# Optimization experiments

Measured on AMD Instinct MI355X. Metric: run time of the kernel, lower is better.

Reference implementation:

```python
import jax, jax.numpy as jnp
import numpy as np

N_EMBD = 384
NUM_HEADS = 6
HEAD_SIZE = 64


def setup_inputs() -> dict:
    key = jax.random.key(0)
    k1, k2, k3, k4 = jax.random.split(key, 4)
    B, T = 32, 1024
    x = jax.random.normal(k1, (B, T, N_EMBD), dtype=jnp.float32)
    # torch Linear(n_embd, 3*n_embd, bias=False): store as [in, out]
    s_attn = 1.0 / np.sqrt(N_EMBD)
    W_attn = jax.random.uniform(k2, (N_EMBD, 3 * N_EMBD), dtype=jnp.float32, minval=-s_attn, maxval=s_attn)
    W_proj = jax.random.uniform(k3, (N_EMBD, N_EMBD), dtype=jnp.float32, minval=-s_attn, maxval=s_attn)
    b_proj = jax.random.uniform(k4, (N_EMBD,), dtype=jnp.float32, minval=-s_attn, maxval=s_attn)
    return {"x": x, "W_attn": W_attn, "W_proj": W_proj, "b_proj": b_proj}


def reference(x, W_attn, W_proj, b_proj):
    B, T, C = x.shape
    H, D = NUM_HEADS, HEAD_SIZE
    qkv = x @ W_attn                      # [B, T, 3C]
    q, k, v = jnp.split(qkv, 3, axis=2)   # each [B, T, C]
    # [B, H, T, D]
    q = q.reshape(B, T, H, D).transpose(0, 2, 1, 3)
    k = k.reshape(B, T, H, D).transpose(0, 2, 1, 3)
    v = v.reshape(B, T, H, D).transpose(0, 2, 1, 3)
    scale = 1.0 / jnp.sqrt(jnp.asarray(D, dtype=x.dtype))
    scores = jnp.einsum("bhqd,bhkd->bhqk", q, k) * scale  # [B, H, T, T]
    causal = jnp.tril(jnp.ones((T, T), dtype=bool))
    scores = jnp.where(causal, scores, jnp.asarray(-jnp.inf, dtype=scores.dtype))
    attn = jax.nn.softmax(scores, axis=-1)
    y = jnp.einsum("bhqk,bhkd->bhqd", attn, v)             # [B, H, T, D]
    y = y.transpose(0, 2, 1, 3).reshape(B, T, C)
    # dropout is inactive in eval mode
    return y @ W_proj + b_proj
```

## Files before the change

### kernel.cpp

```cpp
#include <hip/hip_runtime.h>
#include <hip/hip_bf16.h>

#define DEV __device__ __forceinline__

typedef __attribute__((ext_vector_type(4))) float f32x4;
typedef __bf16 bf16x8 __attribute__((ext_vector_type(8)));

static DEV unsigned short f2bf(float f) {
    union { float f; unsigned u; } x; x.f = f;
    unsigned r = x.u + 0x7fffu + ((x.u >> 16) & 1u);
    return (unsigned short)(r >> 16);
}

static DEV f32x4 zero4() { f32x4 v; v[0] = 0.f; v[1] = 0.f; v[2] = 0.f; v[3] = 0.f; return v; }

#define GL1(p) ((const __attribute__((address_space(1))) void*)(p))
#define LDS3(p) ((__attribute__((address_space(3))) void*)(p))


__global__ __launch_bounds__(256) void k_prep(
    const float* __restrict__ x, unsigned short* __restrict__ xb,
    const float* __restrict__ Wa, unsigned short* __restrict__ WaT,
    const float* __restrict__ Wp, unsigned short* __restrict__ WpT)
{
    int i = blockIdx.x * 256 + threadIdx.x;
    if (i < 3145728) {
        float4 v = reinterpret_cast<const float4*>(x)[i];
        ushort4 o;
        o.x = f2bf(v.x); o.y = f2bf(v.y); o.z = f2bf(v.z); o.w = f2bf(v.w);
        reinterpret_cast<ushort4*>(xb)[i] = o;
    } else if (i < 3145728 + 442368) {
        int j = i - 3145728;
        int n = j / 384, k = j - n * 384;
        WaT[j] = f2bf(Wa[(size_t)k * 1152 + n]);
    } else if (i < 3145728 + 442368 + 147456) {
        int j = i - (3145728 + 442368);
        int n = j / 384, k = j - n * 384;
        WpT[j] = f2bf(Wp[(size_t)k * 384 + n]);
    }
}


template <int SWAP>
static DEV void gemm_mainloop(
    const unsigned short* __restrict__ A,
    const unsigned short* __restrict__ B,
    int m0, int n0, int tid,
    f32x4 (&acc)[4][4],
    unsigned short (&lA)[128][64], unsigned short (&lB)[128][64])
{
    const int K = 384;
    const int w = tid >> 6, lane = tid & 63;
    const int wm = (w >> 1) * 64, wn = (w & 1) * 64;
    const int lr = lane & 15, lg = lane >> 4;
    const int lrow = lane >> 3;
    const int lcol = ((lane & 7) ^ lrow) * 8;

    for (int kb = 0; kb < K; kb += 64) {
        __syncthreads();
#pragma unroll
        for (int c = 0; c < 4; ++c) {
            int rb = (w * 4 + c) * 8;
            __builtin_amdgcn_global_load_lds(GL1(&A[(size_t)(m0 + rb + lrow) * K + kb + lcol]),
                                             LDS3(&lA[rb][0]), 16, 0, 0);
            __builtin_amdgcn_global_load_lds(GL1(&B[(size_t)(n0 + rb + lrow) * K + kb + lcol]),
                                             LDS3(&lB[rb][0]), 16, 0, 0);
        }
        __syncthreads();

        bf16x8 af[4][2], bfr[4][2];
#pragma unroll
        for (int kc = 0; kc < 2; ++kc) {
#pragma unroll
            for (int t = 0; t < 4; ++t) {
                int ga = ((kc * 4 + lg) ^ (lr & 7)) * 8;
                af[t][kc]  = *(const bf16x8*)&lA[wm + t * 16 + lr][ga];
                bfr[t][kc] = *(const bf16x8*)&lB[wn + t * 16 + lr][ga];
            }
        }
#pragma unroll
        for (int kc = 0; kc < 2; ++kc)
#pragma unroll
            for (int mt = 0; mt < 4; ++mt)
#pragma unroll
                for (int nt = 0; nt < 4; ++nt)
                    acc[mt][nt] = SWAP
                        ? __builtin_amdgcn_mfma_f32_16x16x32_bf16(bfr[nt][kc], af[mt][kc], acc[mt][nt], 0, 0, 0)
                        : __builtin_amdgcn_mfma_f32_16x16x32_bf16(af[mt][kc], bfr[nt][kc], acc[mt][nt], 0, 0, 0);
    }
}


__global__ __launch_bounds__(256) void k_gemm_qkv(
    const unsigned short* __restrict__ A,
    const unsigned short* __restrict__ B,
    unsigned short* __restrict__ Qb, unsigned short* __restrict__ Kb,
    unsigned short* __restrict__ Vb)
{
    __shared__ unsigned short lA[128][64];
    __shared__ unsigned short lB[128][64];

    const int bid = blockIdx.x;
    const int xcd = bid & 7, s = bid >> 3;
    const int mi = xcd * 32 + s / 9;
    const int cj = s % 9;
    const int m0 = mi * 128, n0 = cj * 128;

    const int tid = threadIdx.x;
    const int w = tid >> 6, lane = tid & 63;
    const int wm = (w >> 1) * 64, wn = (w & 1) * 64;
    const int lr = lane & 15, lg = lane >> 4;

    f32x4 acc[4][4];
#pragma unroll
    for (int i = 0; i < 4; i++)
#pragma unroll
        for (int j = 0; j < 4; j++) acc[i][j] = zero4();

    if (cj < 6) {
        gemm_mainloop<1>(A, B, m0, n0, tid, acc, lA, lB);
        const int which = cj / 3;
#pragma unroll
        for (int mt = 0; mt < 4; ++mt) {
            int row = m0 + wm + mt * 16 + lr;
            int bb = row >> 10, tloc = row & 1023;
#pragma unroll
            for (int nt = 0; nt < 4; ++nt) {
                int col = n0 + wn + nt * 16 + lg * 4;
                int c = col - which * 384;
                int hh = c >> 6, d0 = c & 63;
                size_t bh = (size_t)bb * 6 + hh;
                int kc = (d0 >> 5) & 1;
                int ln = (tloc & 15) + 16 * ((d0 >> 3) & 3);
                int e0 = d0 & 7;
                union { __bf16 h4[4]; uint2 u; } pk;
                if (which == 0) {
#pragma unroll
                    for (int r = 0; r < 4; ++r)
                        pk.h4[r] = (__bf16)(acc[mt][nt][r] * 0.18033688f);
                    int qt = tloc >> 5, fmt = (tloc >> 4) & 1;
                    *(uint2*)&Qb[((((bh * 32 + qt) * 2 + fmt) * 2 + kc) * 64 + ln) * 8 + e0] = pk.u;
                } else {
#pragma unroll
                    for (int r = 0; r < 4; ++r)
                        pk.h4[r] = (__bf16)acc[mt][nt][r];
                    int ktt = tloc >> 6, fnt = (tloc >> 4) & 3;
                    *(uint2*)&Kb[((((bh * 16 + ktt) * 4 + fnt) * 2 + kc) * 64 + ln) * 8 + e0] = pk.u;
                }
            }
        }
    } else {
        gemm_mainloop<0>(A, B, m0, n0, tid, acc, lA, lB);
#pragma unroll
        for (int nt = 0; nt < 4; ++nt) {
            int col = n0 + wn + nt * 16 + lr;
            int c = col - 768;
            int hh = c >> 6, d = c & 63;
            int fnt = d >> 4;
#pragma unroll
            for (int mt = 0; mt < 4; ++mt) {
                int row0 = m0 + wm + mt * 16 + lg * 4;
                int bb = row0 >> 10, t0 = row0 & 1023;
                size_t bh = (size_t)bb * 6 + hh;
                int ktt = t0 >> 6, kc = (t0 >> 5) & 1, e0 = t0 & 7;
                int ln = (d & 15) + 16 * ((t0 >> 3) & 3);
                union { __bf16 h4[4]; uint2 u; } pk;
#pragma unroll
                for (int r = 0; r < 4; ++r)
                    pk.h4[r] = (__bf16)acc[mt][nt][r];
                *(uint2*)&Vb[((((bh * 16 + ktt) * 4 + fnt) * 2 + kc) * 64 + ln) * 8 + e0] = pk.u;
            }
        }
    }
}


__global__ __launch_bounds__(256) void k_gemm_proj(
    const unsigned short* __restrict__ A,
    const unsigned short* __restrict__ B,
    const float* __restrict__ bias, float* __restrict__ Out)
{
    __shared__ unsigned short lA[128][64];
    __shared__ unsigned short lB[128][64];

    const int bid = blockIdx.x;
    const int xcd = bid & 7, s = bid >> 3;
    const int mi = xcd * 32 + s / 3;
    const int cj = s % 3;
    const int m0 = mi * 128, n0 = cj * 128;

    const int tid = threadIdx.x;
    const int w = tid >> 6, lane = tid & 63;
    const int wm = (w >> 1) * 64, wn = (w & 1) * 64;
    const int lr = lane & 15, lg = lane >> 4;

    f32x4 acc[4][4];
#pragma unroll
    for (int i = 0; i < 4; i++)
#pragma unroll
        for (int j = 0; j < 4; j++) acc[i][j] = zero4();

    gemm_mainloop<1>(A, B, m0, n0, tid, acc, lA, lB);

#pragma unroll
    for (int mt = 0; mt < 4; ++mt) {
        int row = m0 + wm + mt * 16 + lr;
#pragma unroll
        for (int nt = 0; nt < 4; ++nt) {
            int col = n0 + wn + nt * 16 + lg * 4;
            f32x4 bv = *(const f32x4*)&bias[col];
            f32x4 ov;
#pragma unroll
            for (int r = 0; r < 4; ++r) ov[r] = acc[mt][nt][r] + bv[r];
            *(f32x4*)&Out[(size_t)row * 384 + col] = ov;
        }
    }
}


template <int NTM, bool MASK>
static DEV void attn_qtile(
    const bf16x8 (&kf)[4][2], const bf16x8 (&vf)[4][2],
    const bf16x8 (&qf)[2][2], f32x4 (&o)[2][4], float (&ls)[2],
    unsigned short* lPw, int kt, int qw, int lr, int lg)
{
    constexpr int KCM = NTM / 2;

    f32x4 st[2][NTM];
#pragma unroll
    for (int mt = 0; mt < 2; ++mt)
#pragma unroll
        for (int nt = 0; nt < NTM; ++nt) st[mt][nt] = zero4();

    __builtin_amdgcn_s_setprio(1);
#pragma unroll
    for (int kc = 0; kc < 2; ++kc)
#pragma unroll
        for (int mt = 0; mt < 2; ++mt)
#pragma unroll
            for (int nt = 0; nt < NTM; ++nt)
                st[mt][nt] = __builtin_amdgcn_mfma_f32_16x16x32_bf16(kf[nt][kc], qf[mt][kc], st[mt][nt], 0, 0, 0);
    __builtin_amdgcn_s_setprio(0);

#pragma unroll
    for (int mt = 0; mt < 2; ++mt) {
#pragma unroll
        for (int nt = 0; nt < NTM; ++nt) {
            union { __bf16 hh[4]; uint2 u; } pk;
            float e[4];
#pragma unroll
            for (int r = 0; r < 4; ++r) {
                float ev = __builtin_amdgcn_exp2f(st[mt][nt][r]);
                if (MASK) {
                    int kg = kt * 64 + nt * 16 + lg * 4 + r;
                    int qg = qw + mt * 16 + lr;
                    if (kg > qg) ev = 0.f;
                }
                e[r] = ev;
                pk.hh[r] = (__bf16)ev;
            }
            ls[mt] += (e[0] + e[1]) + (e[2] + e[3]);
            int ln2 = lr + 16 * ((nt & 1) * 2 + (lg >> 1));
            *(uint2*)&lPw[(mt * 2 + (nt >> 1)) * 512 + ln2 * 8 + (lg & 1) * 4] = pk.u;
        }
    }

    bf16x8 pf[2][KCM];
#pragma unroll
    for (int mt = 0; mt < 2; ++mt)
#pragma unroll
        for (int kc = 0; kc < KCM; ++kc)
            pf[mt][kc] = *(const bf16x8*)&lPw[(mt * 2 + kc) * 512 + (lr + 16 * lg) * 8];

    __builtin_amdgcn_s_setprio(1);
#pragma unroll
    for (int mt = 0; mt < 2; ++mt)
#pragma unroll
        for (int nt = 0; nt < 4; ++nt)
#pragma unroll
            for (int kc = 0; kc < KCM; ++kc)
                o[mt][nt] = __builtin_amdgcn_mfma_f32_16x16x32_bf16(vf[nt][kc], pf[mt][kc], o[mt][nt], 0, 0, 0);
    __builtin_amdgcn_s_setprio(0);
}

static DEV void attn_out(const f32x4 (&o)[2][4], const float (&ls)[2],
                         int qw, int b, int h, int lr, int lg,
                         unsigned short* __restrict__ Y)
{
    float inv[2];
#pragma unroll
    for (int mt = 0; mt < 2; ++mt) {
        float s = ls[mt];
        s += __shfl_xor(s, 16);
        s += __shfl_xor(s, 32);
        inv[mt] = 1.0f / s;
    }
#pragma unroll
    for (int mt = 0; mt < 2; ++mt) {
#pragma unroll
        for (int nt = 0; nt < 4; ++nt) {
            union { __bf16 h4[4]; uint2 u; } pk;
#pragma unroll
            for (int r = 0; r < 4; ++r) pk.h4[r] = (__bf16)(o[mt][nt][r] * inv[mt]);
            *(uint2*)&Y[((size_t)b * 1024 + qw + mt * 16 + lr) * 384 + h * 64 + nt * 16 + lg * 4] = pk.u;
        }
    }
}

__global__ __launch_bounds__(256, 2) void k_attn(
    const unsigned short* __restrict__ Qf,
    const unsigned short* __restrict__ Kf,
    const unsigned short* __restrict__ Vf,
    unsigned short* __restrict__ Y)
{
    __shared__ unsigned short lK[2][4096];
    __shared__ unsigned short lV[2][4096];
    __shared__ unsigned short lPf[4][2048];

    const int tid = threadIdx.x;
    const int w = tid >> 6, lane = tid & 63;
    const int lr = lane & 15, lg = lane >> 4;
    const int bh = blockIdx.x;
    const int pg = 3 - blockIdx.y;
    const int p = 4 * pg + w;
    const int qtA = 2 * p, qtB = 2 * p + 1;
    const int qwA = qtA * 32, qwB = qtB * 32;
    const int nkt = p + 1;
    const int nsteps = 4 * pg + 4;
    const int b = bh / 6, h = bh - b * 6;

    const unsigned short* Kbh = Kf + (size_t)bh * 65536;
    const unsigned short* Vbh = Vf + (size_t)bh * 65536;

    bf16x8 qfA[2][2], qfB[2][2];
#pragma unroll
    for (int mt = 0; mt < 2; ++mt)
#pragma unroll
        for (int kc = 0; kc < 2; ++kc) {
            qfA[mt][kc] = *(const bf16x8*)&Qf[((((size_t)bh * 32 + qtA) * 2 + mt) * 2 + kc) * 512 + lane * 8];
            qfB[mt][kc] = *(const bf16x8*)&Qf[((((size_t)bh * 32 + qtB) * 2 + mt) * 2 + kc) * 512 + lane * 8];
        }

    f32x4 oA[2][4], oB[2][4];
    float lsA[2] = {0.f, 0.f}, lsB[2] = {0.f, 0.f};
#pragma unroll
    for (int mt = 0; mt < 2; ++mt)
#pragma unroll
        for (int nt = 0; nt < 4; ++nt) { oA[mt][nt] = zero4(); oB[mt][nt] = zero4(); }

#pragma unroll
    for (int i = 0; i < 2; ++i) {
        __builtin_amdgcn_global_load_lds(GL1(Kbh + (size_t)w * 1024 + i * 512 + lane * 8),
                                         LDS3(&lK[0][w * 1024 + i * 512]), 16, 0, 0);
        __builtin_amdgcn_global_load_lds(GL1(Vbh + (size_t)w * 1024 + i * 512 + lane * 8),
                                         LDS3(&lV[0][w * 1024 + i * 512]), 16, 0, 0);
    }

    for (int kt = 0; kt < nsteps; ++kt) {
        __syncthreads();
        if (kt + 1 < nsteps) {
            int nb = (kt + 1) & 1;
#pragma unroll
            for (int i = 0; i < 2; ++i) {
                __builtin_amdgcn_global_load_lds(GL1(Kbh + (size_t)(kt + 1) * 4096 + w * 1024 + i * 512 + lane * 8),
                                                 LDS3(&lK[nb][w * 1024 + i * 512]), 16, 0, 0);
                __builtin_amdgcn_global_load_lds(GL1(Vbh + (size_t)(kt + 1) * 4096 + w * 1024 + i * 512 + lane * 8),
                                                 LDS3(&lV[nb][w * 1024 + i * 512]), 16, 0, 0);
            }
        }
        if (kt < nkt) {
            const unsigned short* lKt = lK[kt & 1];
            const unsigned short* lVt = lV[kt & 1];

            bf16x8 kf[4][2], vf[4][2];
#pragma unroll
            for (int nt = 0; nt < 4; ++nt)
#pragma unroll
                for (int kc = 0; kc < 2; ++kc) {
                    kf[nt][kc] = *(const bf16x8*)&lKt[(nt * 2 + kc) * 512 + lane * 8];
                    vf[nt][kc] = *(const bf16x8*)&lVt[(nt * 2 + kc) * 512 + lane * 8];
                }

            if (kt == nkt - 1) {
                attn_qtile<2, true>(kf, vf, qfA, oA, lsA, lPf[w], kt, qwA, lr, lg);
                attn_qtile<4, true>(kf, vf, qfB, oB, lsB, lPf[w], kt, qwB, lr, lg);
            } else {
                attn_qtile<4, false>(kf, vf, qfA, oA, lsA, lPf[w], kt, qwA, lr, lg);
                attn_qtile<4, false>(kf, vf, qfB, oB, lsB, lPf[w], kt, qwB, lr, lg);
            }
        }
    }

    attn_out(oA, lsA, qwA, b, h, lr, lg, Y);
    attn_out(oB, lsB, qwB, b, h, lr, lg, Y);
}


extern "C" void kernel_launch(void* const* d_in, const int* in_sizes, int n_in,
                              void* d_out, int out_size, void* d_ws, size_t ws_size,
                              hipStream_t stream)
{
    const float* x  = (const float*)d_in[0];
    const float* Wa = (const float*)d_in[1];
    const float* Wp = (const float*)d_in[2];
    const float* bp = (const float*)d_in[3];
    float* out = (float*)d_out;

    char* ws = (char*)d_ws;
    unsigned short* xb  = (unsigned short*)(ws);
    unsigned short* WaT = (unsigned short*)(ws + 25165824);
    unsigned short* WpT = (unsigned short*)(ws + 26050560);
    unsigned short* Qb  = (unsigned short*)(ws + 26345472);
    unsigned short* Kb  = (unsigned short*)(ws + 51511296);
    unsigned short* Vtb = (unsigned short*)(ws + 76677120);

    k_prep<<<14592, 256, 0, stream>>>(x, xb, Wa, WaT, Wp, WpT);
    k_gemm_qkv<<<2304, 256, 0, stream>>>(xb, WaT, Qb, Kb, Vtb);
    k_attn<<<dim3(192, 4), 256, 0, stream>>>(Qb, Kb, Vtb, xb);
    k_gemm_proj<<<768, 256, 0, stream>>>(xb, WpT, bp, out);
}
```

Before: 126.8 us.

## Pair light and heavy causal query groups per attention block for load balance

The attention kernel now launches half as many blocks. Each block runs two phases: one over query group p and one over the mirrored group 15-p, so every block does about the same causal work. This is meant to remove the tail imbalance where blocks over late query tiles process many more key tiles than blocks over early ones. In exchange each block runs longer and serially, there are fewer blocks to hide latency, and an extra barrier and pipeline restart sit between the phases.

```diff
diff --git a/kernel.cpp b/kernel.cpp
--- a/kernel.cpp
+++ b/kernel.cpp
@@ -307,6 +307,85 @@
     }
 }
 
+static DEV void attn_phase(
+    int p, int nstage, int w, int lane, int b, int h, int bh,
+    const unsigned short* __restrict__ Qf,
+    const unsigned short* __restrict__ Kbh,
+    const unsigned short* __restrict__ Vbh,
+    unsigned short* __restrict__ Y,
+    unsigned short (&lK)[2][4096], unsigned short (&lV)[2][4096],
+    unsigned short* lPw)
+{
+    const int lr = lane & 15, lg = lane >> 4;
+    const int qtA = 2 * p, qtB = 2 * p + 1;
+    const int qwA = qtA * 32, qwB = qtB * 32;
+    const int nkt = p + 1;
+
+    bf16x8 qfA[2][2], qfB[2][2];
+#pragma unroll
+    for (int mt = 0; mt < 2; ++mt)
+#pragma unroll
+        for (int kc = 0; kc < 2; ++kc) {
+            qfA[mt][kc] = *(const bf16x8*)&Qf[((((size_t)bh * 32 + qtA) * 2 + mt) * 2 + kc) * 512 + lane * 8];
+            qfB[mt][kc] = *(const bf16x8*)&Qf[((((size_t)bh * 32 + qtB) * 2 + mt) * 2 + kc) * 512 + lane * 8];
+        }
+
+    f32x4 oA[2][4], oB[2][4];
+    float lsA[2] = {0.f, 0.f}, lsB[2] = {0.f, 0.f};
+#pragma unroll
+    for (int mt = 0; mt < 2; ++mt)
+#pragma unroll
+        for (int nt = 0; nt < 4; ++nt) { oA[mt][nt] = zero4(); oB[mt][nt] = zero4(); }
+
+    __syncthreads();
+
+#pragma unroll
+    for (int i = 0; i < 2; ++i) {
+        __builtin_amdgcn_global_load_lds(GL1(Kbh + (size_t)w * 1024 + i * 512 + lane * 8),
+                                         LDS3(&lK[0][w * 1024 + i * 512]), 16, 0, 0);
+        __builtin_amdgcn_global_load_lds(GL1(Vbh + (size_t)w * 1024 + i * 512 + lane * 8),
+                                         LDS3(&lV[0][w * 1024 + i * 512]), 16, 0, 0);
+    }
+
+    for (int kt = 0; kt < nstage; ++kt) {
+        __syncthreads();
+        if (kt + 1 < nstage) {
+            int nb = (kt + 1) & 1;
+#pragma unroll
+            for (int i = 0; i < 2; ++i) {
+                __builtin_amdgcn_global_load_lds(GL1(Kbh + (size_t)(kt + 1) * 4096 + w * 1024 + i * 512 + lane * 8),
+                                                 LDS3(&lK[nb][w * 1024 + i * 512]), 16, 0, 0);
+                __builtin_amdgcn_global_load_lds(GL1(Vbh + (size_t)(kt + 1) * 4096 + w * 1024 + i * 512 + lane * 8),
+                                                 LDS3(&lV[nb][w * 1024 + i * 512]), 16, 0, 0);
+            }
+        }
+        if (kt < nkt) {
+            const unsigned short* lKt = lK[kt & 1];
+            const unsigned short* lVt = lV[kt & 1];
+
+            bf16x8 kf[4][2], vf[4][2];
+#pragma unroll
+            for (int nt = 0; nt < 4; ++nt)
+#pragma unroll
+                for (int kc = 0; kc < 2; ++kc) {
+                    kf[nt][kc] = *(const bf16x8*)&lKt[(nt * 2 + kc) * 512 + lane * 8];
+                    vf[nt][kc] = *(const bf16x8*)&lVt[(nt * 2 + kc) * 512 + lane * 8];
+                }
+
+            if (kt == nkt - 1) {
+                attn_qtile<2, true>(kf, vf, qfA, oA, lsA, lPw, kt, qwA, lr, lg);
+                attn_qtile<4, true>(kf, vf, qfB, oB, lsB, lPw, kt, qwB, lr, lg);
+            } else {
+                attn_qtile<4, false>(kf, vf, qfA, oA, lsA, lPw, kt, qwA, lr, lg);
+                attn_qtile<4, false>(kf, vf, qfB, oB, lsB, lPw, kt, qwB, lr, lg);
+            }
+        }
+    }
+
+    attn_out(oA, lsA, qwA, b, h, lr, lg, Y);
+    attn_out(oB, lsB, qwB, b, h, lr, lg, Y);
+}
+
 __global__ __launch_bounds__(256, 2) void k_attn(
     const unsigned short* __restrict__ Qf,
     const unsigned short* __restrict__ Kf,
@@ -319,80 +398,16 @@
 
     const int tid = threadIdx.x;
     const int w = tid >> 6, lane = tid & 63;
-    const int lr = lane & 15, lg = lane >> 4;
     const int bh = blockIdx.x;
-    const int pg = 3 - blockIdx.y;
-    const int p = 4 * pg + w;
-    const int qtA = 2 * p, qtB = 2 * p + 1;
-    const int qwA = qtA * 32, qwB = qtB * 32;
-    const int nkt = p + 1;
-    const int nsteps = 4 * pg + 4;
+    const int y = blockIdx.y;
     const int b = bh / 6, h = bh - b * 6;
 
     const unsigned short* Kbh = Kf + (size_t)bh * 65536;
     const unsigned short* Vbh = Vf + (size_t)bh * 65536;
 
-    bf16x8 qfA[2][2], qfB[2][2];
-#pragma unroll
-    for (int mt = 0; mt < 2; ++mt)
-#pragma unroll
-        for (int kc = 0; kc < 2; ++kc) {
-            qfA[mt][kc] = *(const bf16x8*)&Qf[((((size_t)bh * 32 + qtA) * 2 + mt) * 2 + kc) * 512 + lane * 8];
-            qfB[mt][kc] = *(const bf16x8*)&Qf[((((size_t)bh * 32 + qtB) * 2 + mt) * 2 + kc) * 512 + lane * 8];
-        }
-
-    f32x4 oA[2][4], oB[2][4];
-    float lsA[2] = {0.f, 0.f}, lsB[2] = {0.f, 0.f};
-#pragma unroll
-    for (int mt = 0; mt < 2; ++mt)
-#pragma unroll
-        for (int nt = 0; nt < 4; ++nt) { oA[mt][nt] = zero4(); oB[mt][nt] = zero4(); }
-
-#pragma unroll
-    for (int i = 0; i < 2; ++i) {
-        __builtin_amdgcn_global_load_lds(GL1(Kbh + (size_t)w * 1024 + i * 512 + lane * 8),
-                                         LDS3(&lK[0][w * 1024 + i * 512]), 16, 0, 0);
-        __builtin_amdgcn_global_load_lds(GL1(Vbh + (size_t)w * 1024 + i * 512 + lane * 8),
-                                         LDS3(&lV[0][w * 1024 + i * 512]), 16, 0, 0);
-    }
-
-    for (int kt = 0; kt < nsteps; ++kt) {
-        __syncthreads();
-        if (kt + 1 < nsteps) {
-            int nb = (kt + 1) & 1;
-#pragma unroll
-            for (int i = 0; i < 2; ++i) {
-                __builtin_amdgcn_global_load_lds(GL1(Kbh + (size_t)(kt + 1) * 4096 + w * 1024 + i * 512 + lane * 8),
-                                                 LDS3(&lK[nb][w * 1024 + i * 512]), 16, 0, 0);
-                __builtin_amdgcn_global_load_lds(GL1(Vbh + (size_t)(kt + 1) * 4096 + w * 1024 + i * 512 + lane * 8),
-                                                 LDS3(&lV[nb][w * 1024 + i * 512]), 16, 0, 0);
-            }
-        }
-        if (kt < nkt) {
-            const unsigned short* lKt = lK[kt & 1];
-            const unsigned short* lVt = lV[kt & 1];
-
-            bf16x8 kf[4][2], vf[4][2];
-#pragma unroll
-            for (int nt = 0; nt < 4; ++nt)
-#pragma unroll
-                for (int kc = 0; kc < 2; ++kc) {
-                    kf[nt][kc] = *(const bf16x8*)&lKt[(nt * 2 + kc) * 512 + lane * 8];
-                    vf[nt][kc] = *(const bf16x8*)&lVt[(nt * 2 + kc) * 512 + lane * 8];
-                }
-
-            if (kt == nkt - 1) {
-                attn_qtile<2, true>(kf, vf, qfA, oA, lsA, lPf[w], kt, qwA, lr, lg);
-                attn_qtile<4, true>(kf, vf, qfB, oB, lsB, lPf[w], kt, qwB, lr, lg);
-            } else {
-                attn_qtile<4, false>(kf, vf, qfA, oA, lsA, lPf[w], kt, qwA, lr, lg);
-                attn_qtile<4, false>(kf, vf, qfB, oB, lsB, lPf[w], kt, qwB, lr, lg);
-            }
-        }
-    }
-
-    attn_out(oA, lsA, qwA, b, h, lr, lg, Y);
-    attn_out(oB, lsB, qwB, b, h, lr, lg, Y);
+    const int pA = 4 * y + w;
+    attn_phase(pA,      4 * y + 4,  w, lane, b, h, bh, Qf, Kbh, Vbh, Y, lK, lV, lPf[w]);
+    attn_phase(15 - pA, 16 - 4 * y, w, lane, b, h, bh, Qf, Kbh, Vbh, Y, lK, lV, lPf[w]);
 }
 
 
@@ -416,6 +431,6 @@
 
     k_prep<<<14592, 256, 0, stream>>>(x, xb, Wa, WaT, Wp, WpT);
     k_gemm_qkv<<<2304, 256, 0, stream>>>(xb, WaT, Qb, Kb, Vtb);
-    k_attn<<<dim3(192, 4), 256, 0, stream>>>(Qb, Kb, Vtb, xb);
+    k_attn<<<dim3(192, 2), 256, 0, stream>>>(Qb, Kb, Vtb, xb);
     k_gemm_proj<<<768, 256, 0, stream>>>(xb, WpT, bp, out);
 }
```

New measurement: 132.7 us. 4.6% more time.
